# Kernel tuning notes

Measured on AMD Instinct MI355X. Metric: run time of the kernel, lower is better.

The kernel has to match this reference:

```python
import jax, jax.numpy as jnp
import numpy as np

N_NODES = 100000
N_GRAPHS = 64

def gcn_conv(x, edge_index, W, b, num_nodes):
    # PyG GCNConv: x' = D^-1/2 (A + I) D^-1/2 (x W) + b
    h = x @ W  # [N, out]
    row, col = edge_index[0], edge_index[1]
    loops = jnp.arange(num_nodes, dtype=row.dtype)
    src = jnp.concatenate([row, loops])  # message source (x_j)
    dst = jnp.concatenate([col, loops])  # aggregation target
    deg = jax.ops.segment_sum(jnp.ones_like(src, dtype=h.dtype), dst,
                              num_segments=num_nodes)
    dinv = jnp.where(deg > 0, jax.lax.rsqrt(deg), 0.0)
    norm = dinv[src] * dinv[dst]  # [E+N]
    msgs = h[src] * norm[:, None]  # gather-transform
    out = jax.ops.segment_sum(msgs, dst, num_segments=num_nodes)  # scatter
    return out + b

def global_mean_pool(x, batch, num_graphs):
    sums = jax.ops.segment_sum(x, batch, num_segments=num_graphs)
    cnts = jax.ops.segment_sum(jnp.ones((x.shape[0],), x.dtype), batch,
                               num_segments=num_graphs)
    return sums / jnp.maximum(cnts, 1.0)[:, None]

def setup_inputs() -> dict:
    key = jax.random.key(0)
    ks = jax.random.split(key, 12)
    d_in, d_hid, d_mid, d_out = 128, 128, 20, 10
    n_edges = 1600000
    x = jax.random.normal(ks[0], (N_NODES, d_in), dtype=jnp.float32)
    edge_index = jax.random.randint(ks[1], (2, n_edges), 0, N_NODES, dtype=jnp.int64)
    batch = jnp.sort(jax.random.randint(ks[2], (N_NODES,), 0, N_GRAPHS, dtype=jnp.int64))
    def glorot(k, fan_in, fan_out):
        s = (6.0 / (fan_in + fan_out)) ** 0.5
        return jax.random.uniform(k, (fan_in, fan_out), jnp.float32, -s, s)
    return {
        "x": x, "edge_index": edge_index, "batch": batch,
        "W1": glorot(ks[3], d_in, d_hid), "b1": jnp.zeros((d_hid,), jnp.float32),
        "W2": glorot(ks[4], d_hid, d_hid), "b2": jnp.zeros((d_hid,), jnp.float32),
        "fc1_W": glorot(ks[5], d_hid, d_mid), "fc1_b": jnp.zeros((d_mid,), jnp.float32),
        "fc2_W": glorot(ks[6], d_mid, d_out), "fc2_b": jnp.zeros((d_out,), jnp.float32),
    }

def reference(x, edge_index, batch, W1, b1, W2, b2, fc1_W, fc1_b, fc2_W, fc2_b):
    # eval mode: dropout is identity
    h = gcn_conv(x, edge_index, W1, b1, N_NODES)
    h = jax.nn.elu(h)
    h = gcn_conv(h, edge_index, W2, b2, N_NODES)
    g = global_mean_pool(h, batch, N_GRAPHS)  # [G, hidden]
    g = jax.nn.relu(g @ fc1_W + fc1_b)
    g = g @ fc2_W + fc2_b
    return jax.nn.log_softmax(g, axis=1)
```

## Files before the change

kernel.cpp:

```cpp
#include <hip/hip_runtime.h>
#include <math.h>

#define DH 128
#define BCAP 16384

typedef __bf16 bf8_t __attribute__((ext_vector_type(8)));
typedef short short8 __attribute__((ext_vector_type(8)));
typedef float f4_t __attribute__((ext_vector_type(4)));
typedef float f2_t __attribute__((ext_vector_type(2)));

__device__ inline unsigned short f2b(float f) {
    unsigned int u = __builtin_bit_cast(unsigned int, f);
    u = u + 0x7fffu + ((u >> 16) & 1u);
    return (unsigned short)(u >> 16);
}
__device__ inline float b2f(unsigned short h) {
    return __builtin_bit_cast(float, (unsigned int)h << 16);
}

__global__ __launch_bounds__(256) void k_bucket(const int* __restrict__ row,
                                                const int* __restrict__ col,
                                                int E, int nbuck, int chunk,
                                                unsigned int* __restrict__ pairs,
                                                int* __restrict__ bcur) {
    __shared__ int lcnt[256];
    __shared__ int lbase[256];
    __shared__ unsigned int srec[8192];
    int t = threadIdx.x;
    int e0 = blockIdx.x * chunk;
    int e1 = min(e0 + chunk, E);
    lcnt[t] = 0;
    __syncthreads();
    for (int i = e0 + t; i < e1; i += 256) {
        int d = col[i];
        int b = d >> 9;
        int slot = atomicAdd(&lcnt[b], 1);
        srec[i - e0] = ((unsigned int)b << 22) | ((unsigned int)(d & 511) << 13)
                     | (unsigned int)slot;
    }
    __syncthreads();
    if (t < nbuck) {
        int c = lcnt[t];
        lbase[t] = (c > 0) ? atomicAdd(&bcur[t * 16], c) : 0;
    }
    __syncthreads();
    for (int i = e0 + t; i < e1; i += 256) {
        unsigned int r = srec[i - e0];
        int b = r >> 22;
        unsigned int dl = (r >> 13) & 511u;
        int slot = (int)(r & 8191u);
        int g = lbase[b] + slot;
        if (g < BCAP)
            pairs[(size_t)b * BCAP + g] = ((unsigned int)row[i] << 9) | dl;
    }
}

__global__ __launch_bounds__(256) void k_build(const unsigned int* __restrict__ pairs,
                                               const int* __restrict__ bcur,
                                               int nbuck, int N,
                                               int* __restrict__ off,
                                               float* __restrict__ dinv,
                                               int* __restrict__ csr) {
    __shared__ int sb[256];
    __shared__ int cnt2[512];
    __shared__ int excl[512];
    __shared__ int curi[512];
    __shared__ int stmp[256];
    int b = blockIdx.x, t = threadIdx.x;
    sb[t] = (t < nbuck) ? min(bcur[t * 16], BCAP) : 0;
    __syncthreads();
    for (int d = 1; d < 256; d <<= 1) {
        int v = (t >= d) ? sb[t - d] : 0;
        __syncthreads();
        sb[t] += v;
        __syncthreads();
    }
    int base = (b == 0) ? 0 : sb[b - 1];
    int cnt = sb[b] - base;
    int node0 = b << 9;
    int nodes = min(512, N - node0);
    cnt2[t] = 0; cnt2[t + 256] = 0;
    __syncthreads();
    const unsigned int* pp = pairs + (size_t)b * BCAP;
    for (int i = t; i < cnt; i += 256)
        atomicAdd(&cnt2[pp[i] & 511u], 1);
    __syncthreads();
    stmp[t] = cnt2[2 * t] + cnt2[2 * t + 1];
    __syncthreads();
    for (int d = 1; d < 256; d <<= 1) {
        int v = (t >= d) ? stmp[t - d] : 0;
        __syncthreads();
        stmp[t] += v;
        __syncthreads();
    }
    int pre = (t == 0) ? 0 : stmp[t - 1];
    excl[2 * t] = pre;
    excl[2 * t + 1] = pre + cnt2[2 * t];
    __syncthreads();
    if (t < nodes) {
        off[node0 + t] = base + excl[t];
        dinv[node0 + t] = rsqrtf((float)(cnt2[t] + 1));
    }
    int t2 = t + 256;
    if (t2 < nodes) {
        off[node0 + t2] = base + excl[t2];
        dinv[node0 + t2] = rsqrtf((float)(cnt2[t2] + 1));
    }
    if (t == 0) off[node0 + nodes] = base + cnt;
    curi[t] = excl[t]; curi[t + 256] = excl[t + 256];
    __syncthreads();
    for (int i = t; i < cnt; i += 256) {
        unsigned int p = pp[i];
        int d = (int)(p & 511u);
        int slot = atomicAdd(&curi[d], 1);
        csr[base + slot] = (int)(p >> 9);
    }
}

__global__ void k_prepW(const float* __restrict__ W1, const float* __restrict__ W2,
                        unsigned short* __restrict__ Wt1, unsigned short* __restrict__ Wt2) {
    int t = blockIdx.x * blockDim.x + threadIdx.x;
    int v = t & 16383;
    int k = v >> 7, n = v & 127;
    if (t < 16384) {
        Wt1[n * DH + k] = f2b(W1[k * DH + n]);
    } else {
        int p = ((k & 15) << 3) | (k >> 4);
        Wt2[n * DH + p] = f2b(W2[k * DH + n]);
    }
}

__global__ __launch_bounds__(256) void k_gemm_mfma(const void* __restrict__ Xin, int x_is_bf16,
                                                   const unsigned short* __restrict__ Wt,
                                                   const float* __restrict__ dinv,
                                                   unsigned char* __restrict__ Y, int nrows) {
    __shared__ unsigned short Xs[64 * 136];
    __shared__ unsigned short Ws[128 * 136];
    int t = threadIdx.x;
    int row0 = blockIdx.x * 64;

    for (int v = t; v < 128 * 32; v += 256) {
        int n = v >> 5, kq = v & 31;
        ushort4 w = ((const ushort4*)Wt)[v];
        *(ushort4*)&Ws[n * 136 + kq * 4] = w;
    }
    if (x_is_bf16) {
        const unsigned short* X = (const unsigned short*)Xin;
        for (int v = t; v < 64 * 32; v += 256) {
            int r = v >> 5, cq = v & 31;
            int gr = row0 + r;
            ushort4 h;
            if (gr < nrows) h = ((const ushort4*)X)[(size_t)gr * 32 + cq];
            else { h.x = 0; h.y = 0; h.z = 0; h.w = 0; }
            *(ushort4*)&Xs[r * 136 + cq * 4] = h;
        }
    } else {
        const float* X = (const float*)Xin;
        for (int v = t; v < 64 * 32; v += 256) {
            int r = v >> 5, cq = v & 31;
            int gr = row0 + r;
            ushort4 h;
            if (gr < nrows) {
                float4 xv = ((const float4*)X)[(size_t)gr * 32 + cq];
                h.x = f2b(xv.x); h.y = f2b(xv.y); h.z = f2b(xv.z); h.w = f2b(xv.w);
            } else { h.x = 0; h.y = 0; h.z = 0; h.w = 0; }
            *(ushort4*)&Xs[r * 136 + cq * 4] = h;
        }
    }
    __syncthreads();

    int w = t >> 6;
    int lane = t & 63;
    int quad = lane >> 4;
    int l16 = lane & 15;
    int rw = w * 16;

    f4_t acc[8];
#pragma unroll
    for (int j = 0; j < 8; j++) acc[j] = (f4_t){0.f, 0.f, 0.f, 0.f};

#pragma unroll
    for (int kk = 0; kk < 4; kk++) {
        int k0 = kk * 32;
        bf8_t a = __builtin_bit_cast(bf8_t,
            *(const short8*)&Xs[(rw + l16) * 136 + k0 + quad * 8]);
#pragma unroll
        for (int j = 0; j < 8; j++) {
            bf8_t b = __builtin_bit_cast(bf8_t,
                *(const short8*)&Ws[(j * 16 + l16) * 136 + k0 + quad * 8]);
            acc[j] = __builtin_amdgcn_mfma_f32_16x16x32_bf16(a, b, acc[j], 0, 0, 0);
        }
    }

#pragma unroll
    for (int reg = 0; reg < 4; reg++) {
        int r = row0 + rw + quad * 4 + reg;
        if (r < nrows) {
            float dv = dinv[r];
            float v0 = acc[0][reg] * dv, v1 = acc[1][reg] * dv;
            float v2 = acc[2][reg] * dv, v3 = acc[3][reg] * dv;
            float v4 = acc[4][reg] * dv, v5 = acc[5][reg] * dv;
            float v6 = acc[6][reg] * dv, v7 = acc[7][reg] * dv;
            int d0 = __builtin_amdgcn_cvt_pk_fp8_f32(v0, v1, 0, false);
            d0 = __builtin_amdgcn_cvt_pk_fp8_f32(v2, v3, d0, true);
            int d1 = __builtin_amdgcn_cvt_pk_fp8_f32(v4, v5, 0, false);
            d1 = __builtin_amdgcn_cvt_pk_fp8_f32(v6, v7, d1, true);
            *(uint2*)&Y[(size_t)r * DH + l16 * 8] = make_uint2((unsigned)d0, (unsigned)d1);
        }
    }
}

__global__ __launch_bounds__(256) void k_agg(const unsigned char* __restrict__ T,
                                             unsigned short* __restrict__ Out,
                                             const float* __restrict__ dinv,
                                             const int* __restrict__ off,
                                             const int* __restrict__ csr,
                                             const float* __restrict__ bias,
                                             int elu, int N) {
    __shared__ int ofs[17];
    __shared__ int sidx[768];
    int t = threadIdx.x;
    int d0 = blockIdx.x * 16;
    if (t < 17) ofs[t] = off[min(d0 + t, N)];
    __syncthreads();
    int s0 = ofs[0];
    int cnt = ofs[16] - s0;
    int scnt = min(cnt, 768);
    for (int k = t; k < scnt; k += 256) sidx[k] = csr[s0 + k];
    __syncthreads();

    int w = t >> 6;
    int lane = t & 63;
    int half = lane >> 5;
    int l5 = lane & 31;
    const unsigned char* Tl = T + (l5 << 2);

    for (int ni = 0; ni < 4; ni++) {
        int nd = d0 + 4 * w + ni;
        if (nd >= N) break;
        int eL = ofs[4 * w + ni] - s0;
        int eH = ofs[4 * w + ni + 1] - s0;
        int deg = eH - eL;

        float a0, a1, a2, a3;
        {
            unsigned int u = *(const unsigned int*)(Tl + ((size_t)nd << 7));
            if (half) u = 0;
            f2_t lo = __builtin_amdgcn_cvt_pk_f32_fp8(u, false);
            f2_t hi = __builtin_amdgcn_cvt_pk_f32_fp8(u, true);
            a0 = lo[0]; a1 = lo[1]; a2 = hi[0]; a3 = hi[1];
        }

        if (eH <= scnt) {
            int base_e = eL + half;
            int Pf = deg >> 1;
            int P4 = Pf & ~3;
            int i = 0;
            for (; i < P4; i += 4) {
                int ea = base_e + 2 * i;
                int j0 = sidx[ea];
                int j1 = sidx[ea + 2];
                int j2 = sidx[ea + 4];
                int j3 = sidx[ea + 6];
                unsigned int u0 = *(const unsigned int*)(Tl + ((size_t)j0 << 7));
                unsigned int u1 = *(const unsigned int*)(Tl + ((size_t)j1 << 7));
                unsigned int u2 = *(const unsigned int*)(Tl + ((size_t)j2 << 7));
                unsigned int u3 = *(const unsigned int*)(Tl + ((size_t)j3 << 7));
                f2_t lo0 = __builtin_amdgcn_cvt_pk_f32_fp8(u0, false);
                f2_t hi0 = __builtin_amdgcn_cvt_pk_f32_fp8(u0, true);
                f2_t lo1 = __builtin_amdgcn_cvt_pk_f32_fp8(u1, false);
                f2_t hi1 = __builtin_amdgcn_cvt_pk_f32_fp8(u1, true);
                f2_t lo2 = __builtin_amdgcn_cvt_pk_f32_fp8(u2, false);
                f2_t hi2 = __builtin_amdgcn_cvt_pk_f32_fp8(u2, true);
                f2_t lo3 = __builtin_amdgcn_cvt_pk_f32_fp8(u3, false);
                f2_t hi3 = __builtin_amdgcn_cvt_pk_f32_fp8(u3, true);
                a0 += (lo0[0] + lo1[0]) + (lo2[0] + lo3[0]);
                a1 += (lo0[1] + lo1[1]) + (lo2[1] + lo3[1]);
                a2 += (hi0[0] + hi1[0]) + (hi2[0] + hi3[0]);
                a3 += (hi0[1] + hi1[1]) + (hi2[1] + hi3[1]);
            }
            for (; i < Pf; i++) {
                int j0 = sidx[base_e + 2 * i];
                unsigned int u0 = *(const unsigned int*)(Tl + ((size_t)j0 << 7));
                f2_t lo = __builtin_amdgcn_cvt_pk_f32_fp8(u0, false);
                f2_t hi = __builtin_amdgcn_cvt_pk_f32_fp8(u0, true);
                a0 += lo[0]; a1 += lo[1]; a2 += hi[0]; a3 += hi[1];
            }
            if (deg & 1) {
                int j0 = sidx[eL + deg - 1];
                unsigned int u0 = *(const unsigned int*)(Tl + ((size_t)j0 << 7));
                if (half) u0 = 0;
                f2_t lo = __builtin_amdgcn_cvt_pk_f32_fp8(u0, false);
                f2_t hi = __builtin_amdgcn_cvt_pk_f32_fp8(u0, true);
                a0 += lo[0]; a1 += lo[1]; a2 += hi[0]; a3 += hi[1];
            }
        } else {
            int gb = s0 + eL + half;
            int Pf = deg >> 1;
            for (int i = 0; i < Pf; i++) {
                int j0 = csr[gb + 2 * i];
                unsigned int u0 = *(const unsigned int*)(Tl + ((size_t)j0 << 7));
                f2_t lo = __builtin_amdgcn_cvt_pk_f32_fp8(u0, false);
                f2_t hi = __builtin_amdgcn_cvt_pk_f32_fp8(u0, true);
                a0 += lo[0]; a1 += lo[1]; a2 += hi[0]; a3 += hi[1];
            }
            if (deg & 1) {
                int j0 = csr[s0 + eL + deg - 1];
                unsigned int u0 = *(const unsigned int*)(Tl + ((size_t)j0 << 7));
                if (half) u0 = 0;
                f2_t lo = __builtin_amdgcn_cvt_pk_f32_fp8(u0, false);
                f2_t hi = __builtin_amdgcn_cvt_pk_f32_fp8(u0, true);
                a0 += lo[0]; a1 += lo[1]; a2 += hi[0]; a3 += hi[1];
            }
        }

        a0 += __shfl_xor(a0, 32);
        a1 += __shfl_xor(a1, 32);
        a2 += __shfl_xor(a2, 32);
        a3 += __shfl_xor(a3, 32);

        if (!half) {
            float dv = dinv[nd];
            int c0 = ((l5 & 1) << 6) | (l5 >> 1);
            float o0 = a0 * dv + bias[c0];
            float o1 = a1 * dv + bias[c0 + 16];
            float o2 = a2 * dv + bias[c0 + 32];
            float o3 = a3 * dv + bias[c0 + 48];
            if (elu) {
                o0 = o0 > 0.f ? o0 : expm1f(o0);
                o1 = o1 > 0.f ? o1 : expm1f(o1);
                o2 = o2 > 0.f ? o2 : expm1f(o2);
                o3 = o3 > 0.f ? o3 : expm1f(o3);
            }
            unsigned int p0 = (unsigned int)f2b(o0) | ((unsigned int)f2b(o1) << 16);
            unsigned int p1 = (unsigned int)f2b(o2) | ((unsigned int)f2b(o3) << 16);
            *(uint2*)&Out[(size_t)nd * DH + (l5 << 2)] = make_uint2(p0, p1);
        }
    }
}

__global__ __launch_bounds__(256) void k_pool(const unsigned int* __restrict__ H32,
                                              const int* __restrict__ batch,
                                              float* __restrict__ Gsum,
                                              int* __restrict__ cnts, int N) {
    int g = blockIdx.x;
    int p = blockIdx.y;
    int t = threadIdx.x;
    int lane = t & 63;
    int rg = t >> 6;
    int lo = 0, hi = N;
    while (lo < hi) { int m = (lo + hi) >> 1; if (batch[m] < g) lo = m + 1; else hi = m; }
    int s = lo;
    hi = N;
    while (lo < hi) { int m = (lo + hi) >> 1; if (batch[m] < g + 1) lo = m + 1; else hi = m; }
    int e = lo;
    int len = e - s;
    int parts = (int)gridDim.y;
    int chunk = (len + parts - 1) / parts;
    int i0 = s + p * chunk;
    int i1 = min(i0 + chunk, e);
    float a0 = 0.f, a1 = 0.f;
    for (int i = i0 + rg; i < i1; i += 4) {
        unsigned int v = H32[(size_t)i * 64 + lane];
        a0 += b2f((unsigned short)(v & 0xffffu));
        a1 += b2f((unsigned short)(v >> 16));
    }
    __shared__ float ps[4][DH];
    ps[rg][lane * 2] = a0;
    ps[rg][lane * 2 + 1] = a1;
    __syncthreads();
    if (t < DH) {
        float v = ps[0][t] + ps[1][t] + ps[2][t] + ps[3][t];
        atomicAdd(&Gsum[g * DH + t], v);
    }
    if (p == 0 && t == 0) cnts[g] = len;
}

__global__ __launch_bounds__(64) void k_head(const float* __restrict__ Gsum,
                                             const int* __restrict__ cnts,
                                             const float* __restrict__ W1,
                                             const float* __restrict__ b1,
                                             const float* __restrict__ W2,
                                             const float* __restrict__ b2,
                                             float* __restrict__ out) {
    int g = blockIdx.x;
    int t = threadIdx.x;
    __shared__ float gv[DH];
    __shared__ float mid[20];
    __shared__ float o[10];
    float inv = 1.f / fmaxf((float)cnts[g], 1.f);
    for (int i = t; i < DH; i += 64) {
        int c = ((i & 7) << 4) | (i >> 3);
        gv[c] = Gsum[g * DH + i] * inv;
    }
    __syncthreads();
    if (t < 20) {
        float a = b1[t];
        for (int k = 0; k < DH; k++) a += gv[k] * W1[k * 20 + t];
        mid[t] = fmaxf(a, 0.f);
    }
    __syncthreads();
    if (t < 10) {
        float a = b2[t];
        for (int k = 0; k < 20; k++) a += mid[k] * W2[k * 10 + t];
        o[t] = a;
    }
    __syncthreads();
    if (t == 0) {
        float m = -1e30f;
        for (int j = 0; j < 10; j++) m = fmaxf(m, o[j]);
        float ssum = 0.f;
        for (int j = 0; j < 10; j++) ssum += expf(o[j] - m);
        float l = logf(ssum);
        for (int j = 0; j < 10; j++) out[g * 10 + j] = o[j] - m - l;
    }
}

extern "C" void kernel_launch(void* const* d_in, const int* in_sizes, int n_in,
                              void* d_out, int out_size, void* d_ws, size_t ws_size,
                              hipStream_t stream) {
    const float* x    = (const float*)d_in[0];
    const int*   ei   = (const int*)d_in[1];
    const int*   batch= (const int*)d_in[2];
    const float* W1   = (const float*)d_in[3];
    const float* b1   = (const float*)d_in[4];
    const float* W2   = (const float*)d_in[5];
    const float* b2   = (const float*)d_in[6];
    const float* fc1W = (const float*)d_in[7];
    const float* fc1b = (const float*)d_in[8];
    const float* fc2W = (const float*)d_in[9];
    const float* fc2b = (const float*)d_in[10];
    float* out = (float*)d_out;

    int N = in_sizes[0] / DH;
    int E = in_sizes[1] / 2;
    int G = out_size / 10;

    char* p = (char*)d_ws;
    auto alloc = [&](size_t bytes) {
        char* r = p;
        p += (bytes + 255) & ~(size_t)255;
        return r;
    };
    unsigned char*  t8 = (unsigned char*)alloc((size_t)N * DH);
    unsigned short* a1 = (unsigned short*)alloc((size_t)N * DH * 2);
    int*   csr  = (int*)alloc((size_t)E * 4);
    int*   off  = (int*)alloc((size_t)(N + 1) * 4);
    float* dinv = (float*)alloc((size_t)N * 4);
    int nbuck = (N + 511) >> 9;
    unsigned int* pairs = (unsigned int*)alloc((size_t)nbuck * BCAP * 4);
    unsigned short* Wt1 = (unsigned short*)alloc(DH * DH * 2);
    unsigned short* Wt2 = (unsigned short*)alloc(DH * DH * 2);
    float* Gsum = (float*)alloc((size_t)G * DH * 4);
    int*   bcur = (int*)alloc(256 * 16 * 4);
    int*   cnts = (int*)alloc((size_t)G * 4);

    const int* row = ei;
    const int* col = ei + E;

    (void)hipMemsetAsync(Gsum, 0, (size_t)G * DH * 4 + 256 * 16 * 4, stream);

    const int chunk = 8192;
    int ablocks = (E + chunk - 1) / chunk;
    k_bucket<<<ablocks, 256, 0, stream>>>(row, col, E, nbuck, chunk, pairs, bcur);
    k_build<<<nbuck, 256, 0, stream>>>(pairs, bcur, nbuck, N, off, dinv, csr);
    k_prepW<<<128, 256, 0, stream>>>(W1, W2, Wt1, Wt2);

    int gblocks = (N + 63) / 64;
    int mblocks = (N + 15) / 16;
    k_gemm_mfma<<<gblocks, 256, 0, stream>>>(x, 0, Wt1, dinv, t8, N);
    k_agg<<<mblocks, 256, 0, stream>>>(t8, a1, dinv, off, csr, b1, 1, N);
    k_gemm_mfma<<<gblocks, 256, 0, stream>>>(a1, 1, Wt2, dinv, t8, N);
    k_agg<<<mblocks, 256, 0, stream>>>(t8, a1, dinv, off, csr, b2, 0, N);

    dim3 pg(G, 32);
    k_pool<<<pg, 256, 0, stream>>>((const unsigned int*)a1, batch, Gsum, cnts, N);
    k_head<<<G, 64, 0, stream>>>(Gsum, cnts, fc1W, fc1b, fc2W, fc2b, out);
}
```

Before: 312.1 us.

## Pad per-node CSR rows to multiples of 16 with dummy zero row; unroll aggregation

Builds a padded CSR where each node's neighbor list is rounded up to 16 entries, filled with an index pointing at an extra zeroed row of the fp8 feature table. This lets the aggregation run branch-free 8-wide gathers with no remainder or odd-degree tails. Aggregation now uses one node per wave with 4 nodes per block, and the global bucket prefix scan is dropped by using fixed per-bucket CSR bases. It also aliases the pairs buffer with t8 and swaps expm1f for __expf-1. In exchange it does extra gathers of the dummy row, uses more CSR memory, and loses a little ELU accuracy near zero.

```diff
diff --git a/kernel.cpp b/kernel.cpp
--- a/kernel.cpp
+++ b/kernel.cpp
@@ -59,24 +59,17 @@
                                                const int* __restrict__ bcur,
                                                int nbuck, int N,
                                                int* __restrict__ off,
+                                               int* __restrict__ dpd,
                                                float* __restrict__ dinv,
                                                int* __restrict__ csr) {
-    __shared__ int sb[256];
     __shared__ int cnt2[512];
+    __shared__ int pd2[512];
     __shared__ int excl[512];
     __shared__ int curi[512];
     __shared__ int stmp[256];
     int b = blockIdx.x, t = threadIdx.x;
-    sb[t] = (t < nbuck) ? min(bcur[t * 16], BCAP) : 0;
-    __syncthreads();
-    for (int d = 1; d < 256; d <<= 1) {
-        int v = (t >= d) ? sb[t - d] : 0;
-        __syncthreads();
-        sb[t] += v;
-        __syncthreads();
-    }
-    int base = (b == 0) ? 0 : sb[b - 1];
-    int cnt = sb[b] - base;
+    int cnt = min(bcur[b * 16], BCAP);
+    int base = b * BCAP;
     int node0 = b << 9;
     int nodes = min(512, N - node0);
     cnt2[t] = 0; cnt2[t + 256] = 0;
@@ -85,7 +78,10 @@
     for (int i = t; i < cnt; i += 256)
         atomicAdd(&cnt2[pp[i] & 511u], 1);
     __syncthreads();
-    stmp[t] = cnt2[2 * t] + cnt2[2 * t + 1];
+    pd2[t] = (cnt2[t] + 15) & ~15;
+    pd2[t + 256] = (cnt2[t + 256] + 15) & ~15;
+    __syncthreads();
+    stmp[t] = pd2[2 * t] + pd2[2 * t + 1];
     __syncthreads();
     for (int d = 1; d < 256; d <<= 1) {
         int v = (t >= d) ? stmp[t - d] : 0;
@@ -95,25 +91,31 @@
     }
     int pre = (t == 0) ? 0 : stmp[t - 1];
     excl[2 * t] = pre;
-    excl[2 * t + 1] = pre + cnt2[2 * t];
+    excl[2 * t + 1] = pre + pd2[2 * t];
     __syncthreads();
     if (t < nodes) {
         off[node0 + t] = base + excl[t];
+        dpd[node0 + t] = pd2[t];
         dinv[node0 + t] = rsqrtf((float)(cnt2[t] + 1));
     }
     int t2 = t + 256;
     if (t2 < nodes) {
         off[node0 + t2] = base + excl[t2];
+        dpd[node0 + t2] = pd2[t2];
         dinv[node0 + t2] = rsqrtf((float)(cnt2[t2] + 1));
     }
-    if (t == 0) off[node0 + nodes] = base + cnt;
     curi[t] = excl[t]; curi[t + 256] = excl[t + 256];
     __syncthreads();
     for (int i = t; i < cnt; i += 256) {
         unsigned int p = pp[i];
         int d = (int)(p & 511u);
         int slot = atomicAdd(&curi[d], 1);
-        csr[base + slot] = (int)(p >> 9);
+        if (slot < BCAP) csr[base + slot] = (int)(p >> 9);
+    }
+    for (int n = t; n < 512; n += 256) {
+        int e0 = excl[n] + cnt2[n];
+        int e1 = min(excl[n] + pd2[n], BCAP);
+        for (int k = e0; k < e1; k++) csr[base + k] = N;
     }
 }
 
@@ -210,22 +212,63 @@
     }
 }
 
+#define AGG_ROUND(IDX)                                                     \
+    {                                                                      \
+        int ea = be + 2 * i;                                               \
+        int j0 = IDX(ea);      int j1 = IDX(ea + 2);                       \
+        int j2 = IDX(ea + 4);  int j3 = IDX(ea + 6);                       \
+        int j4 = IDX(ea + 8);  int j5 = IDX(ea + 10);                      \
+        int j6 = IDX(ea + 12); int j7 = IDX(ea + 14);                      \
+        unsigned int u0 = Tw[(j0 << 5) + l5];                              \
+        unsigned int u1 = Tw[(j1 << 5) + l5];                              \
+        unsigned int u2 = Tw[(j2 << 5) + l5];                              \
+        unsigned int u3 = Tw[(j3 << 5) + l5];                              \
+        unsigned int u4 = Tw[(j4 << 5) + l5];                              \
+        unsigned int u5 = Tw[(j5 << 5) + l5];                              \
+        unsigned int u6 = Tw[(j6 << 5) + l5];                              \
+        unsigned int u7 = Tw[(j7 << 5) + l5];                              \
+        accA01 += __builtin_amdgcn_cvt_pk_f32_fp8(u0, false);              \
+        accA23 += __builtin_amdgcn_cvt_pk_f32_fp8(u0, true);               \
+        accB01 += __builtin_amdgcn_cvt_pk_f32_fp8(u1, false);              \
+        accB23 += __builtin_amdgcn_cvt_pk_f32_fp8(u1, true);               \
+        accA01 += __builtin_amdgcn_cvt_pk_f32_fp8(u2, false);              \
+        accA23 += __builtin_amdgcn_cvt_pk_f32_fp8(u2, true);               \
+        accB01 += __builtin_amdgcn_cvt_pk_f32_fp8(u3, false);              \
+        accB23 += __builtin_amdgcn_cvt_pk_f32_fp8(u3, true);               \
+        accA01 += __builtin_amdgcn_cvt_pk_f32_fp8(u4, false);              \
+        accA23 += __builtin_amdgcn_cvt_pk_f32_fp8(u4, true);               \
+        accB01 += __builtin_amdgcn_cvt_pk_f32_fp8(u5, false);              \
+        accB23 += __builtin_amdgcn_cvt_pk_f32_fp8(u5, true);               \
+        accA01 += __builtin_amdgcn_cvt_pk_f32_fp8(u6, false);              \
+        accA23 += __builtin_amdgcn_cvt_pk_f32_fp8(u6, true);               \
+        accB01 += __builtin_amdgcn_cvt_pk_f32_fp8(u7, false);              \
+        accB23 += __builtin_amdgcn_cvt_pk_f32_fp8(u7, true);               \
+    }
+
 __global__ __launch_bounds__(256) void k_agg(const unsigned char* __restrict__ T,
                                              unsigned short* __restrict__ Out,
                                              const float* __restrict__ dinv,
                                              const int* __restrict__ off,
+                                             const int* __restrict__ dpd,
                                              const int* __restrict__ csr,
                                              const float* __restrict__ bias,
                                              int elu, int N) {
-    __shared__ int ofs[17];
-    __shared__ int sidx[768];
+    __shared__ int ofs[4];
+    __shared__ int dps[4];
+    __shared__ float dv4[4];
+    __shared__ int sidx[320];
     int t = threadIdx.x;
-    int d0 = blockIdx.x * 16;
-    if (t < 17) ofs[t] = off[min(d0 + t, N)];
+    int d0 = blockIdx.x * 4;
+    if (t < 4) {
+        int n = min(d0 + t, N - 1);
+        ofs[t] = off[n];
+        dps[t] = dpd[n];
+        dv4[t] = dinv[n];
+    }
     __syncthreads();
     int s0 = ofs[0];
-    int cnt = ofs[16] - s0;
-    int scnt = min(cnt, 768);
+    int span = ofs[3] + dps[3] - s0;
+    int scnt = min(span, 320);
     for (int k = t; k < scnt; k += 256) sidx[k] = csr[s0 + k];
     __syncthreads();
 
@@ -233,104 +276,56 @@
     int lane = t & 63;
     int half = lane >> 5;
     int l5 = lane & 31;
-    const unsigned char* Tl = T + (l5 << 2);
-
-    for (int ni = 0; ni < 4; ni++) {
-        int nd = d0 + 4 * w + ni;
-        if (nd >= N) break;
-        int eL = ofs[4 * w + ni] - s0;
-        int eH = ofs[4 * w + ni + 1] - s0;
-        int deg = eH - eL;
-
-        float a0, a1, a2, a3;
+    const unsigned int* Tw = (const unsigned int*)T;
+
+    int nd = d0 + w;
+    if (nd < N) {
+        int eL = ofs[w] - s0;
+        int pdw = dps[w];
+        int K = pdw >> 1;
+
+        f2_t accA01, accA23;
+        f2_t accB01 = (f2_t){0.f, 0.f}, accB23 = (f2_t){0.f, 0.f};
         {
-            unsigned int u = *(const unsigned int*)(Tl + ((size_t)nd << 7));
+            unsigned int u = Tw[(nd << 5) + l5];
             if (half) u = 0;
-            f2_t lo = __builtin_amdgcn_cvt_pk_f32_fp8(u, false);
-            f2_t hi = __builtin_amdgcn_cvt_pk_f32_fp8(u, true);
-            a0 = lo[0]; a1 = lo[1]; a2 = hi[0]; a3 = hi[1];
-        }
-
-        if (eH <= scnt) {
-            int base_e = eL + half;
-            int Pf = deg >> 1;
-            int P4 = Pf & ~3;
-            int i = 0;
-            for (; i < P4; i += 4) {
-                int ea = base_e + 2 * i;
-                int j0 = sidx[ea];
-                int j1 = sidx[ea + 2];
-                int j2 = sidx[ea + 4];
-                int j3 = sidx[ea + 6];
-                unsigned int u0 = *(const unsigned int*)(Tl + ((size_t)j0 << 7));
-                unsigned int u1 = *(const unsigned int*)(Tl + ((size_t)j1 << 7));
-                unsigned int u2 = *(const unsigned int*)(Tl + ((size_t)j2 << 7));
-                unsigned int u3 = *(const unsigned int*)(Tl + ((size_t)j3 << 7));
-                f2_t lo0 = __builtin_amdgcn_cvt_pk_f32_fp8(u0, false);
-                f2_t hi0 = __builtin_amdgcn_cvt_pk_f32_fp8(u0, true);
-                f2_t lo1 = __builtin_amdgcn_cvt_pk_f32_fp8(u1, false);
-                f2_t hi1 = __builtin_amdgcn_cvt_pk_f32_fp8(u1, true);
-                f2_t lo2 = __builtin_amdgcn_cvt_pk_f32_fp8(u2, false);
-                f2_t hi2 = __builtin_amdgcn_cvt_pk_f32_fp8(u2, true);
-                f2_t lo3 = __builtin_amdgcn_cvt_pk_f32_fp8(u3, false);
-                f2_t hi3 = __builtin_amdgcn_cvt_pk_f32_fp8(u3, true);
-                a0 += (lo0[0] + lo1[0]) + (lo2[0] + lo3[0]);
-                a1 += (lo0[1] + lo1[1]) + (lo2[1] + lo3[1]);
-                a2 += (hi0[0] + hi1[0]) + (hi2[0] + hi3[0]);
-                a3 += (hi0[1] + hi1[1]) + (hi2[1] + hi3[1]);
-            }
-            for (; i < Pf; i++) {
-                int j0 = sidx[base_e + 2 * i];
-                unsigned int u0 = *(const unsigned int*)(Tl + ((size_t)j0 << 7));
-                f2_t lo = __builtin_amdgcn_cvt_pk_f32_fp8(u0, false);
-                f2_t hi = __builtin_amdgcn_cvt_pk_f32_fp8(u0, true);
-                a0 += lo[0]; a1 += lo[1]; a2 += hi[0]; a3 += hi[1];
-            }
-            if (deg & 1) {
-                int j0 = sidx[eL + deg - 1];
-                unsigned int u0 = *(const unsigned int*)(Tl + ((size_t)j0 << 7));
-                if (half) u0 = 0;
-                f2_t lo = __builtin_amdgcn_cvt_pk_f32_fp8(u0, false);
-                f2_t hi = __builtin_amdgcn_cvt_pk_f32_fp8(u0, true);
-                a0 += lo[0]; a1 += lo[1]; a2 += hi[0]; a3 += hi[1];
-            }
+            accA01 = __builtin_amdgcn_cvt_pk_f32_fp8(u, false);
+            accA23 = __builtin_amdgcn_cvt_pk_f32_fp8(u, true);
+        }
+
+        int be = eL + half;
+        if (eL + pdw <= scnt) {
+#define IDX_L(e) sidx[e]
+            for (int i = 0; i < K; i += 8) AGG_ROUND(IDX_L)
+#undef IDX_L
         } else {
-            int gb = s0 + eL + half;
-            int Pf = deg >> 1;
-            for (int i = 0; i < Pf; i++) {
-                int j0 = csr[gb + 2 * i];
-                unsigned int u0 = *(const unsigned int*)(Tl + ((size_t)j0 << 7));
-                f2_t lo = __builtin_amdgcn_cvt_pk_f32_fp8(u0, false);
-                f2_t hi = __builtin_amdgcn_cvt_pk_f32_fp8(u0, true);
-                a0 += lo[0]; a1 += lo[1]; a2 += hi[0]; a3 += hi[1];
-            }
-            if (deg & 1) {
-                int j0 = csr[s0 + eL + deg - 1];
-                unsigned int u0 = *(const unsigned int*)(Tl + ((size_t)j0 << 7));
-                if (half) u0 = 0;
-                f2_t lo = __builtin_amdgcn_cvt_pk_f32_fp8(u0, false);
-                f2_t hi = __builtin_amdgcn_cvt_pk_f32_fp8(u0, true);
-                a0 += lo[0]; a1 += lo[1]; a2 += hi[0]; a3 += hi[1];
-            }
-        }
-
+            const int* gp = csr + s0;
+#define IDX_G(e) gp[e]
+            for (int i = 0; i < K; i += 8) AGG_ROUND(IDX_G)
+#undef IDX_G
+        }
+
+        float a0 = accA01[0] + accB01[0];
+        float a1 = accA01[1] + accB01[1];
+        float a2 = accA23[0] + accB23[0];
+        float a3 = accA23[1] + accB23[1];
         a0 += __shfl_xor(a0, 32);
         a1 += __shfl_xor(a1, 32);
         a2 += __shfl_xor(a2, 32);
         a3 += __shfl_xor(a3, 32);
 
         if (!half) {
-            float dv = dinv[nd];
             int c0 = ((l5 & 1) << 6) | (l5 >> 1);
+            float dv = dv4[w];
             float o0 = a0 * dv + bias[c0];
             float o1 = a1 * dv + bias[c0 + 16];
             float o2 = a2 * dv + bias[c0 + 32];
             float o3 = a3 * dv + bias[c0 + 48];
             if (elu) {
-                o0 = o0 > 0.f ? o0 : expm1f(o0);
-                o1 = o1 > 0.f ? o1 : expm1f(o1);
-                o2 = o2 > 0.f ? o2 : expm1f(o2);
-                o3 = o3 > 0.f ? o3 : expm1f(o3);
+                o0 = o0 > 0.f ? o0 : __expf(o0) - 1.f;
+                o1 = o1 > 0.f ? o1 : __expf(o1) - 1.f;
+                o2 = o2 > 0.f ? o2 : __expf(o2) - 1.f;
+                o3 = o3 > 0.f ? o3 : __expf(o3) - 1.f;
             }
             unsigned int p0 = (unsigned int)f2b(o0) | ((unsigned int)f2b(o1) << 16);
             unsigned int p1 = (unsigned int)f2b(o2) | ((unsigned int)f2b(o3) << 16);
@@ -435,6 +430,7 @@
     int N = in_sizes[0] / DH;
     int E = in_sizes[1] / 2;
     int G = out_size / 10;
+    int nbuck = (N + 511) >> 9;
 
     char* p = (char*)d_ws;
     auto alloc = [&](size_t bytes) {
@@ -442,13 +438,16 @@
         p += (bytes + 255) & ~(size_t)255;
         return r;
     };
-    unsigned char*  t8 = (unsigned char*)alloc((size_t)N * DH);
+    size_t pairs_bytes = (size_t)nbuck * BCAP * 4;
+    size_t t8_bytes = (size_t)(N + 1) * DH;
+    char* region = alloc(pairs_bytes > t8_bytes ? pairs_bytes : t8_bytes);
+    unsigned int*   pairs = (unsigned int*)region;
+    unsigned char*  t8    = (unsigned char*)region;
     unsigned short* a1 = (unsigned short*)alloc((size_t)N * DH * 2);
-    int*   csr  = (int*)alloc((size_t)E * 4);
-    int*   off  = (int*)alloc((size_t)(N + 1) * 4);
+    int*   csr  = (int*)alloc((size_t)nbuck * BCAP * 4);
+    int*   off  = (int*)alloc((size_t)N * 4);
+    int*   dpd  = (int*)alloc((size_t)N * 4);
     float* dinv = (float*)alloc((size_t)N * 4);
-    int nbuck = (N + 511) >> 9;
-    unsigned int* pairs = (unsigned int*)alloc((size_t)nbuck * BCAP * 4);
     unsigned short* Wt1 = (unsigned short*)alloc(DH * DH * 2);
     unsigned short* Wt2 = (unsigned short*)alloc(DH * DH * 2);
     float* Gsum = (float*)alloc((size_t)G * DH * 4);
@@ -463,15 +462,16 @@
     const int chunk = 8192;
     int ablocks = (E + chunk - 1) / chunk;
     k_bucket<<<ablocks, 256, 0, stream>>>(row, col, E, nbuck, chunk, pairs, bcur);
-    k_build<<<nbuck, 256, 0, stream>>>(pairs, bcur, nbuck, N, off, dinv, csr);
+    k_build<<<nbuck, 256, 0, stream>>>(pairs, bcur, nbuck, N, off, dpd, dinv, csr);
+    (void)hipMemsetAsync(t8 + (size_t)N * DH, 0, DH, stream);
     k_prepW<<<128, 256, 0, stream>>>(W1, W2, Wt1, Wt2);
 
     int gblocks = (N + 63) / 64;
-    int mblocks = (N + 15) / 16;
+    int mblocks = (N + 3) / 4;
     k_gemm_mfma<<<gblocks, 256, 0, stream>>>(x, 0, Wt1, dinv, t8, N);
-    k_agg<<<mblocks, 256, 0, stream>>>(t8, a1, dinv, off, csr, b1, 1, N);
+    k_agg<<<mblocks, 256, 0, stream>>>(t8, a1, dinv, off, dpd, csr, b1, 1, N);
     k_gemm_mfma<<<gblocks, 256, 0, stream>>>(a1, 1, Wt2, dinv, t8, N);
-    k_agg<<<mblocks, 256, 0, stream>>>(t8, a1, dinv, off, csr, b2, 0, N);
+    k_agg<<<mblocks, 256, 0, stream>>>(t8, a1, dinv, off, dpd, csr, b2, 0, N);
 
     dim3 pg(G, 32);
     k_pool<<<pg, 256, 0, stream>>>((const unsigned int*)a1, batch, Gsum, cnts, N);
```

Result: no change. 317.6 us (+1.7%).
